# Optimization experiments

Hardware: AMD Instinct MI355X
Metric: run time of the kernel (lower is better)

The kernel has to match this reference:

```python
import jax, jax.numpy as jnp
import numpy as np

N, M, D = 1024, 1024, 256

def setup_inputs() -> dict:
    key = jax.random.key(0)
    ks = jax.random.split(key, 10)
    s = 1.0 / np.sqrt(D)
    return {
        "f_r": jax.random.normal(ks[0], (N, D), jnp.float32),
        "f_r_prime": jax.random.normal(ks[1], (M, D), jnp.float32),
        "W_w": jax.random.uniform(ks[2], (D, D), jnp.float32, -s, s),
        "W_b": jax.random.uniform(ks[3], (D,), jnp.float32, -s, s),
        "Wp_w": jax.random.uniform(ks[4], (D, D), jnp.float32, -s, s),
        "Wp_b": jax.random.uniform(ks[5], (D,), jnp.float32, -s, s),
        "w_w": jax.random.uniform(ks[6], (1, D), jnp.float32, -s, s),
        "w_b": jax.random.uniform(ks[7], (1,), jnp.float32, -s, s),
        "wp_w": jax.random.uniform(ks[8], (1, D), jnp.float32, -s, s),
        "wp_b": jax.random.uniform(ks[9], (1,), jnp.float32, -s, s),
    }

def reference(f_r, f_r_prime, W_w, W_b, Wp_w, Wp_b, w_w, w_b, wp_w, wp_b):
    q = f_r @ W_w.T + W_b            # [N, D]
    k = f_r_prime @ Wp_w.T + Wp_b    # [M, D]
    # additive (Bahdanau) scores: tanh over broadcast sum [N, M, D]
    h = jnp.tanh(q[:, None, :] + k[None, :, :])
    alpha = h @ w_w.T + w_b          # [N, M, 1]
    alpha = jax.nn.softmax(alpha, axis=1)
    # stage-1 pooling over M (weights on raw f_r_prime, as in source)
    context = jnp.sum(alpha * f_r_prime[None, :, :], axis=1)  # [N, D]
    # stage-2 attention pooling over N
    alpha_p = jax.nn.softmax(context @ wp_w.T + wp_b, axis=0)  # [N, 1]
    pool = jnp.sum(alpha_p * context, axis=0, keepdims=True)   # [1, D]
    return pool
```

## Files before the change

### kernel.cpp

```cpp
#include <hip/hip_runtime.h>

#define NN 1024
#define MM 1024
#define DD 256

typedef float floatx2 __attribute__((ext_vector_type(2)));

__device__ __forceinline__ float rcp_fast(float x) { return __builtin_amdgcn_rcpf(x); }

__global__ __launch_bounds__(256) void gemm_exp_kernel(
    const float* __restrict__ f_r,  const float* __restrict__ W_w,  const float* __restrict__ W_b,
    const float* __restrict__ f_rp, const float* __restrict__ Wp_w, const float* __restrict__ Wp_b,
    const float* __restrict__ wp_w,
    float* __restrict__ Eq, float* __restrict__ EkT, float* __restrict__ g,
    float* __restrict__ out0)
{
    __shared__ float As[32][36];
    __shared__ float Bs[32][68];
    __shared__ float T[64][36];

    const int b = blockIdx.x;
    const int t = threadIdx.x;

    if (b >= 256) {
        const int gb = b - 256;
        if (gb == 0) out0[t] = 0.f;
        const int m = gb * 256 + t;
        const float4* fm = (const float4*)(f_rp + (size_t)m * DD);
        const float4* wp = (const float4*)wp_w;
        float a0 = 0.f, a1 = 0.f, a2 = 0.f, a3 = 0.f;
        #pragma unroll 8
        for (int j = 0; j < 64; ++j) {
            float4 v = fm[j], w = wp[j];
            a0 = fmaf(v.x, w.x, a0); a1 = fmaf(v.y, w.y, a1);
            a2 = fmaf(v.z, w.z, a2); a3 = fmaf(v.w, w.w, a3);
        }
        g[m] = (a0 + a1) + (a2 + a3);
        return;
    }

    const int mat  = b >> 7;
    const int tile = b & 127;
    const int rt = tile & 31, dt = tile >> 5;
    const float* __restrict__ A    = mat ? f_rp : f_r;
    const float* __restrict__ B    = mat ? Wp_w : W_w;
    const float* __restrict__ bias = mat ? Wp_b : W_b;

    const int tx = t & 15, ty = t >> 4;
    const int r0 = rt * 32, d0 = dt * 64;
    const int ar = t >> 3, ak = (t & 7) * 4;
    const int br = t >> 2, bk = (t & 3) * 8;

    float acc[2][4];
    #pragma unroll
    for (int i = 0; i < 2; ++i)
        #pragma unroll
        for (int j = 0; j < 4; ++j) acc[i][j] = 0.f;

    for (int kk = 0; kk < DD; kk += 32) {
        float4 av  = *(const float4*)(A + (size_t)(r0 + ar) * DD + kk + ak);
        float4 bv0 = *(const float4*)(B + (size_t)(d0 + br) * DD + kk + bk);
        float4 bv1 = *(const float4*)(B + (size_t)(d0 + br) * DD + kk + bk + 4);
        __syncthreads();
        As[ak + 0][ar] = av.x; As[ak + 1][ar] = av.y; As[ak + 2][ar] = av.z; As[ak + 3][ar] = av.w;
        Bs[bk + 0][br] = bv0.x; Bs[bk + 1][br] = bv0.y; Bs[bk + 2][br] = bv0.z; Bs[bk + 3][br] = bv0.w;
        Bs[bk + 4][br] = bv1.x; Bs[bk + 5][br] = bv1.y; Bs[bk + 6][br] = bv1.z; Bs[bk + 7][br] = bv1.w;
        __syncthreads();
        #pragma unroll
        for (int k = 0; k < 32; ++k) {
            float2 a2 = *(const float2*)&As[k][ty * 2];
            float4 b4 = *(const float4*)&Bs[k][tx * 4];
            float aa[2] = {a2.x, a2.y};
            float bb[4] = {b4.x, b4.y, b4.z, b4.w};
            #pragma unroll
            for (int i = 0; i < 2; ++i)
                #pragma unroll
                for (int j = 0; j < 4; ++j)
                    acc[i][j] = fmaf(aa[i], bb[j], acc[i][j]);
        }
    }

    float bj[4];
    #pragma unroll
    for (int j = 0; j < 4; ++j) bj[j] = bias[d0 + tx * 4 + j];

    float e[2][4];
    #pragma unroll
    for (int i = 0; i < 2; ++i)
        #pragma unroll
        for (int j = 0; j < 4; ++j) {
            float v = acc[i][j] + bj[j];
            v = fminf(fmaxf(v, -5.f), 5.f);
            e[i][j] = __expf(2.f * v);
        }

    if (mat == 0) {
        #pragma unroll
        for (int i = 0; i < 2; ++i)
            *(float4*)&Eq[(size_t)(r0 + ty * 2 + i) * DD + d0 + tx * 4] =
                make_float4(e[i][0], e[i][1], e[i][2], e[i][3]);
    } else {
        __syncthreads();
        #pragma unroll
        for (int i = 0; i < 2; ++i)
            #pragma unroll
            for (int j = 0; j < 4; ++j) T[tx * 4 + j][ty * 2 + i] = e[i][j];
        __syncthreads();
        const int dl = t >> 3, rl = (t & 7) * 4;
        #pragma unroll
        for (int h = 0; h < 2; ++h) {
            int dloc = dl + 32 * h;
            float4 tv = *(const float4*)&T[dloc][rl];
            *(float4*)&EkT[(size_t)(d0 + dloc) * MM + r0 + rl] = tv;
        }
    }
}

__global__ __launch_bounds__(512, 4) void score_softmax_kernel(
    const float* __restrict__ Eq, const float* __restrict__ EkT,
    const float* __restrict__ w_w, const float* __restrict__ g,
    float* __restrict__ alpha, float* __restrict__ score)
{
    __shared__ float eq[2 * DD];
    __shared__ float w2[DD];
    __shared__ float accbuf[8][256];
    __shared__ float redmx[8 * 2];
    __shared__ float redsm[8 * 2];
    __shared__ float redg[4 * 2];

    const int t  = threadIdx.x;
    const int tg = t >> 8;
    const int tm = t & 255;
    const int lane = t & 63, wid = t >> 6;
    const int n0 = blockIdx.x * 2;
    const int dh = tg * 128;

    eq[t] = Eq[(size_t)n0 * DD + t];
    if (t < DD) w2[t] = -2.0f * w_w[t];
    __syncthreads();

    const floatx2 one2 = {1.f, 1.f};
    floatx2 accl[2] = {{0.f, 0.f}, {0.f, 0.f}};
    floatx2 acch[2] = {{0.f, 0.f}, {0.f, 0.f}};

    const float* ekb = EkT + (size_t)dh * MM + 4 * tm;

    float4 c0 = *(const float4*)(ekb + 0 * MM);
    float4 c1 = *(const float4*)(ekb + 1 * MM);
    float4 c2 = *(const float4*)(ekb + 2 * MM);
    float4 c3 = *(const float4*)(ekb + 3 * MM);

    for (int gi = 0; gi < 32; ++gi) {
        float4 p0 = c0, p1 = c1, p2 = c2, p3 = c3;
        if (gi < 31) {
            const float* nb = ekb + (size_t)(gi * 4 + 4) * MM;
            p0 = *(const float4*)(nb + 0 * MM);
            p1 = *(const float4*)(nb + 1 * MM);
            p2 = *(const float4*)(nb + 2 * MM);
            p3 = *(const float4*)(nb + 3 * MM);
        }
        const int db = gi * 4;
        float4 w4 = *(const float4*)&w2[dh + db];
        float4 qA = *(const float4*)&eq[dh + db];
        float4 qB = *(const float4*)&eq[DD + dh + db];

        floatx2 kv[4][2] = {{{c0.x, c0.y}, {c0.z, c0.w}},
                            {{c1.x, c1.y}, {c1.z, c1.w}},
                            {{c2.x, c2.y}, {c2.z, c2.w}},
                            {{c3.x, c3.y}, {c3.z, c3.w}}};
        float ws[4] = {w4.x, w4.y, w4.z, w4.w};
        float qs[2][4] = {{qA.x, qA.y, qA.z, qA.w}, {qB.x, qB.y, qB.z, qB.w}};

        #pragma unroll
        for (int h = 0; h < 2; ++h) {
            #pragma unroll
            for (int n = 0; n < 2; ++n) {
                floatx2 x0 = qs[n][0] * kv[0][h] + one2;
                floatx2 x1 = qs[n][1] * kv[1][h] + one2;
                floatx2 x2 = qs[n][2] * kv[2][h] + one2;
                floatx2 x3 = qs[n][3] * kv[3][h] + one2;
                floatx2 p01 = x0 * x1;
                floatx2 p23 = x2 * x3;
                floatx2 n01 = ws[0] * x1 + ws[1] * x0;
                floatx2 n23 = ws[2] * x3 + ws[3] * x2;
                floatx2 nc  = n01 * p23 + n23 * p01;
                floatx2 pt  = p01 * p23;
                floatx2 r;  r.x = rcp_fast(pt.x);  r.y = rcp_fast(pt.y);
                if (h == 0) accl[n] += nc * r; else acch[n] += nc * r;
            }
        }
        c0 = p0; c1 = p1; c2 = p2; c3 = p3;
    }

    float acc[2][4];
    #pragma unroll
    for (int n = 0; n < 2; ++n) {
        acc[n][0] = accl[n].x; acc[n][1] = accl[n].y;
        acc[n][2] = acch[n].x; acc[n][3] = acch[n].y;
    }

    if (tg == 1) {
        #pragma unroll
        for (int n = 0; n < 2; ++n)
            #pragma unroll
            for (int j = 0; j < 4; ++j) accbuf[n * 4 + j][tm] = acc[n][j];
    }
    __syncthreads();
    if (tg == 0) {
        #pragma unroll
        for (int n = 0; n < 2; ++n)
            #pragma unroll
            for (int j = 0; j < 4; ++j) acc[n][j] += accbuf[n * 4 + j][tm];
    }

    float mx[2];
    #pragma unroll
    for (int n = 0; n < 2; ++n) {
        mx[n] = (tg == 0) ? fmaxf(fmaxf(acc[n][0], acc[n][1]), fmaxf(acc[n][2], acc[n][3])) : -3e38f;
        #pragma unroll
        for (int off = 32; off > 0; off >>= 1) mx[n] = fmaxf(mx[n], __shfl_xor(mx[n], off));
    }
    if (lane == 0) { redmx[wid * 2] = mx[0]; redmx[wid * 2 + 1] = mx[1]; }
    __syncthreads();
    float MX[2];
    #pragma unroll
    for (int n = 0; n < 2; ++n) {
        float m = redmx[n];
        #pragma unroll
        for (int w = 1; w < 8; ++w) m = fmaxf(m, redmx[w * 2 + n]);
        MX[n] = m;
    }

    float e[2][4], sm[2];
    #pragma unroll
    for (int n = 0; n < 2; ++n) {
        sm[n] = 0.f;
        #pragma unroll
        for (int j = 0; j < 4; ++j) {
            e[n][j] = (tg == 0) ? __expf(acc[n][j] - MX[n]) : 0.f;
            sm[n] += e[n][j];
        }
        #pragma unroll
        for (int off = 32; off > 0; off >>= 1) sm[n] += __shfl_xor(sm[n], off);
    }
    if (lane == 0) { redsm[wid * 2] = sm[0]; redsm[wid * 2 + 1] = sm[1]; }
    __syncthreads();
    if (tg == 0) {
        float4 g4 = *(const float4*)&g[4 * tm];
        float sn[2];
        #pragma unroll
        for (int n = 0; n < 2; ++n) {
            float s = redsm[n];
            #pragma unroll
            for (int w = 1; w < 8; ++w) s += redsm[w * 2 + n];
            float inv = rcp_fast(s);
            float a0 = e[n][0] * inv, a1 = e[n][1] * inv, a2 = e[n][2] * inv, a3 = e[n][3] * inv;
            *(float4*)&alpha[(size_t)(n0 + n) * MM + 4 * tm] = make_float4(a0, a1, a2, a3);
            sn[n] = fmaf(a0, g4.x, fmaf(a1, g4.y, fmaf(a2, g4.z, a3 * g4.w)));
            #pragma unroll
            for (int off = 32; off > 0; off >>= 1) sn[n] += __shfl_xor(sn[n], off);
        }
        if (lane == 0) { redg[wid * 2] = sn[0]; redg[wid * 2 + 1] = sn[1]; }
    }
    __syncthreads();
    if (t == 0) score[n0]     = redg[0] + redg[2] + redg[4] + redg[6];
    if (t == 1) score[n0 + 1] = redg[1] + redg[3] + redg[5] + redg[7];
}

__global__ __launch_bounds__(256) void context_kernel(
    const float* __restrict__ alpha, const float* __restrict__ frp,
    float* __restrict__ part)
{
    __shared__ float als[16][128];
    const int t  = threadIdx.x;
    const int bm = blockIdx.x & 7;
    const int bn = blockIdx.x >> 3;
    const int dq = t & 63;
    const int ng = t >> 6;

    #pragma unroll
    for (int i = 0; i < 2; ++i) {
        int f4i = t + i * 256;
        int row = f4i >> 5, c4 = f4i & 31;
        *(float4*)&als[row][c4 * 4] =
            *(const float4*)&alpha[(size_t)(bn * 16 + row) * MM + bm * 128 + c4 * 4];
    }
    __syncthreads();

    float acc[4][4];
    #pragma unroll
    for (int n = 0; n < 4; ++n)
        #pragma unroll
        for (int j = 0; j < 4; ++j) acc[n][j] = 0.f;

    const float* fb = frp + (size_t)(bm * 128) * DD + 4 * dq;
    for (int m4 = 0; m4 < 32; ++m4) {
        float av[4][4];
        #pragma unroll
        for (int n = 0; n < 4; ++n) {
            float4 a4 = *(const float4*)&als[ng * 4 + n][m4 * 4];
            av[n][0] = a4.x; av[n][1] = a4.y; av[n][2] = a4.z; av[n][3] = a4.w;
        }
        #pragma unroll
        for (int mm = 0; mm < 4; ++mm) {
            float4 f4 = *(const float4*)(fb + (size_t)(m4 * 4 + mm) * DD);
            float fv[4] = {f4.x, f4.y, f4.z, f4.w};
            #pragma unroll
            for (int n = 0; n < 4; ++n)
                #pragma unroll
                for (int j = 0; j < 4; ++j)
                    acc[n][j] = fmaf(av[n][mm], fv[j], acc[n][j]);
        }
    }
    #pragma unroll
    for (int n = 0; n < 4; ++n)
        *(float4*)&part[((size_t)bm << 18) + (size_t)(bn * 16 + ng * 4 + n) * DD + 4 * dq] =
            make_float4(acc[n][0], acc[n][1], acc[n][2], acc[n][3]);
}

__global__ __launch_bounds__(256) void pool_kernel(
    const float* __restrict__ part, const float* __restrict__ score,
    float* __restrict__ out)
{
    __shared__ float red[8];
    const int t = threadIdx.x, lane = t & 63, wid = t >> 6;
    const int n0 = blockIdx.x * 4;

    float s0 = score[t], s1 = score[t + 256], s2 = score[t + 512], s3 = score[t + 768];
    float mx = fmaxf(fmaxf(s0, s1), fmaxf(s2, s3));
    #pragma unroll
    for (int off = 32; off > 0; off >>= 1) mx = fmaxf(mx, __shfl_xor(mx, off));
    if (lane == 0) red[wid] = mx;
    __syncthreads();
    mx = fmaxf(fmaxf(red[0], red[1]), fmaxf(red[2], red[3]));

    float se = __expf(s0 - mx) + __expf(s1 - mx) + __expf(s2 - mx) + __expf(s3 - mx);
    #pragma unroll
    for (int off = 32; off > 0; off >>= 1) se += __shfl_xor(se, off);
    if (lane == 0) red[4 + wid] = se;
    __syncthreads();
    se = red[4] + red[5] + red[6] + red[7];
    float invS = rcp_fast(se);

    float r = 0.f;
    #pragma unroll
    for (int i = 0; i < 4; ++i) {
        float ap = __expf(score[n0 + i] - mx) * invS;
        size_t idx = (size_t)(n0 + i) * DD + t;
        float c = 0.f;
        #pragma unroll
        for (int s = 0; s < 8; ++s) c += part[idx + ((size_t)s << 18)];
        r = fmaf(ap, c, r);
    }
    atomicAdd(out + t, r);
}

extern "C" void kernel_launch(void* const* d_in, const int* in_sizes, int n_in,
                              void* d_out, int out_size, void* d_ws, size_t ws_size,
                              hipStream_t stream) {
    const float* f_r  = (const float*)d_in[0];
    const float* f_rp = (const float*)d_in[1];
    const float* W_w  = (const float*)d_in[2];
    const float* W_b  = (const float*)d_in[3];
    const float* Wp_w = (const float*)d_in[4];
    const float* Wp_b = (const float*)d_in[5];
    const float* w_w  = (const float*)d_in[6];
    const float* wp_w = (const float*)d_in[8];
    float* out = (float*)d_out;

    float* ws    = (float*)d_ws;
    float* Eq    = ws;
    float* EkT   = ws + 262144;
    float* alpha = ws + 524288;
    float* part  = ws + 1572864;
    float* score = ws + 3670016;
    float* g     = ws + 3671040;

    gemm_exp_kernel<<<260, 256, 0, stream>>>(f_r, W_w, W_b, f_rp, Wp_w, Wp_b, wp_w,
                                             Eq, EkT, g, out);
    score_softmax_kernel<<<512, 512, 0, stream>>>(Eq, EkT, w_w, g, alpha, score);
    context_kernel<<<512, 256, 0, stream>>>(alpha, f_rp, part);
    pool_kernel<<<256, 256, 0, stream>>>(part, score, out);
}
```

Before: 136.3 us.

## Fuse score softmax and context pooling into one kernel per four query rows

Merges the score/softmax kernel and the context GEMM kernel into a single 1024-thread kernel. Each block now handles four query rows, keeps alpha in LDS and computes the context rows and the stage-2 scores directly, so the alpha and partial-context buffers no longer round-trip through global memory. The separate g = f_rp·wp_w precompute and one kernel launch are removed. In exchange each block now re-reads all of f_r_prime for only four rows, and the large LDS footprint (over 128KB) limits each CU to one block, which may reduce latency hiding.

```diff
diff --git a/kernel.cpp b/kernel.cpp
--- a/kernel.cpp
+++ b/kernel.cpp
@@ -11,9 +11,7 @@
 __global__ __launch_bounds__(256) void gemm_exp_kernel(
     const float* __restrict__ f_r,  const float* __restrict__ W_w,  const float* __restrict__ W_b,
     const float* __restrict__ f_rp, const float* __restrict__ Wp_w, const float* __restrict__ Wp_b,
-    const float* __restrict__ wp_w,
-    float* __restrict__ Eq, float* __restrict__ EkT, float* __restrict__ g,
-    float* __restrict__ out0)
+    float* __restrict__ Eq, float* __restrict__ EkT, float* __restrict__ out0)
 {
     __shared__ float As[32][36];
     __shared__ float Bs[32][68];
@@ -21,23 +19,7 @@
 
     const int b = blockIdx.x;
     const int t = threadIdx.x;
-
-    if (b >= 256) {
-        const int gb = b - 256;
-        if (gb == 0) out0[t] = 0.f;
-        const int m = gb * 256 + t;
-        const float4* fm = (const float4*)(f_rp + (size_t)m * DD);
-        const float4* wp = (const float4*)wp_w;
-        float a0 = 0.f, a1 = 0.f, a2 = 0.f, a3 = 0.f;
-        #pragma unroll 8
-        for (int j = 0; j < 64; ++j) {
-            float4 v = fm[j], w = wp[j];
-            a0 = fmaf(v.x, w.x, a0); a1 = fmaf(v.y, w.y, a1);
-            a2 = fmaf(v.z, w.z, a2); a3 = fmaf(v.w, w.w, a3);
-        }
-        g[m] = (a0 + a1) + (a2 + a3);
-        return;
-    }
+    if (b == 0) out0[t] = 0.f;
 
     const int mat  = b >> 7;
     const int tile = b & 127;
@@ -116,43 +98,45 @@
     }
 }
 
-__global__ __launch_bounds__(512, 4) void score_softmax_kernel(
+__global__ __launch_bounds__(1024, 4) void fused_attn_kernel(
     const float* __restrict__ Eq, const float* __restrict__ EkT,
-    const float* __restrict__ w_w, const float* __restrict__ g,
-    float* __restrict__ alpha, float* __restrict__ score)
+    const float* __restrict__ w_w, const float* __restrict__ frp,
+    const float* __restrict__ wp_w,
+    float* __restrict__ ctx, float* __restrict__ score)
 {
-    __shared__ float eq[2 * DD];
+    __shared__ float eq[4 * DD];
     __shared__ float w2[DD];
-    __shared__ float accbuf[8][256];
-    __shared__ float redmx[8 * 2];
-    __shared__ float redsm[8 * 2];
-    __shared__ float redg[4 * 2];
+    __shared__ float accbuf[3][16][256];
+    __shared__ float alsm[4][MM];
+    __shared__ float4 ctxred[16][4][64];
+    __shared__ float redmx[4][4];
+    __shared__ float redsm[4][4];
+    __shared__ float redsc[16];
 
     const int t  = threadIdx.x;
     const int tg = t >> 8;
     const int tm = t & 255;
     const int lane = t & 63, wid = t >> 6;
-    const int n0 = blockIdx.x * 2;
-    const int dh = tg * 128;
+    const int n0 = blockIdx.x * 4;
+    const int dh = tg * 64;
 
     eq[t] = Eq[(size_t)n0 * DD + t];
     if (t < DD) w2[t] = -2.0f * w_w[t];
     __syncthreads();
 
     const floatx2 one2 = {1.f, 1.f};
-    floatx2 accl[2] = {{0.f, 0.f}, {0.f, 0.f}};
-    floatx2 acch[2] = {{0.f, 0.f}, {0.f, 0.f}};
+    floatx2 accl[4] = {{0.f,0.f},{0.f,0.f},{0.f,0.f},{0.f,0.f}};
+    floatx2 acch[4] = {{0.f,0.f},{0.f,0.f},{0.f,0.f},{0.f,0.f}};
 
     const float* ekb = EkT + (size_t)dh * MM + 4 * tm;
-
     float4 c0 = *(const float4*)(ekb + 0 * MM);
     float4 c1 = *(const float4*)(ekb + 1 * MM);
     float4 c2 = *(const float4*)(ekb + 2 * MM);
     float4 c3 = *(const float4*)(ekb + 3 * MM);
 
-    for (int gi = 0; gi < 32; ++gi) {
+    for (int gi = 0; gi < 16; ++gi) {
         float4 p0 = c0, p1 = c1, p2 = c2, p3 = c3;
-        if (gi < 31) {
+        if (gi < 15) {
             const float* nb = ekb + (size_t)(gi * 4 + 4) * MM;
             p0 = *(const float4*)(nb + 0 * MM);
             p1 = *(const float4*)(nb + 1 * MM);
@@ -161,28 +145,23 @@
         }
         const int db = gi * 4;
         float4 w4 = *(const float4*)&w2[dh + db];
-        float4 qA = *(const float4*)&eq[dh + db];
-        float4 qB = *(const float4*)&eq[DD + dh + db];
-
         floatx2 kv[4][2] = {{{c0.x, c0.y}, {c0.z, c0.w}},
                             {{c1.x, c1.y}, {c1.z, c1.w}},
                             {{c2.x, c2.y}, {c2.z, c2.w}},
                             {{c3.x, c3.y}, {c3.z, c3.w}}};
-        float ws[4] = {w4.x, w4.y, w4.z, w4.w};
-        float qs[2][4] = {{qA.x, qA.y, qA.z, qA.w}, {qB.x, qB.y, qB.z, qB.w}};
-
-        #pragma unroll
-        for (int h = 0; h < 2; ++h) {
-            #pragma unroll
-            for (int n = 0; n < 2; ++n) {
-                floatx2 x0 = qs[n][0] * kv[0][h] + one2;
-                floatx2 x1 = qs[n][1] * kv[1][h] + one2;
-                floatx2 x2 = qs[n][2] * kv[2][h] + one2;
-                floatx2 x3 = qs[n][3] * kv[3][h] + one2;
+        #pragma unroll
+        for (int n = 0; n < 4; ++n) {
+            float4 q4 = *(const float4*)&eq[n * DD + dh + db];
+            #pragma unroll
+            for (int h = 0; h < 2; ++h) {
+                floatx2 x0 = q4.x * kv[0][h] + one2;
+                floatx2 x1 = q4.y * kv[1][h] + one2;
+                floatx2 x2 = q4.z * kv[2][h] + one2;
+                floatx2 x3 = q4.w * kv[3][h] + one2;
                 floatx2 p01 = x0 * x1;
                 floatx2 p23 = x2 * x3;
-                floatx2 n01 = ws[0] * x1 + ws[1] * x0;
-                floatx2 n23 = ws[2] * x3 + ws[3] * x2;
+                floatx2 n01 = w4.x * x1 + w4.y * x0;
+                floatx2 n23 = w4.z * x3 + w4.w * x2;
                 floatx2 nc  = n01 * p23 + n23 * p01;
                 floatx2 pt  = p01 * p23;
                 floatx2 r;  r.x = rcp_fast(pt.x);  r.y = rcp_fast(pt.y);
@@ -192,134 +171,108 @@
         c0 = p0; c1 = p1; c2 = p2; c3 = p3;
     }
 
-    float acc[2][4];
-    #pragma unroll
-    for (int n = 0; n < 2; ++n) {
+    float acc[4][4];
+    #pragma unroll
+    for (int n = 0; n < 4; ++n) {
         acc[n][0] = accl[n].x; acc[n][1] = accl[n].y;
         acc[n][2] = acch[n].x; acc[n][3] = acch[n].y;
     }
 
-    if (tg == 1) {
-        #pragma unroll
-        for (int n = 0; n < 2; ++n)
-            #pragma unroll
-            for (int j = 0; j < 4; ++j) accbuf[n * 4 + j][tm] = acc[n][j];
+    if (tg > 0) {
+        #pragma unroll
+        for (int n = 0; n < 4; ++n)
+            #pragma unroll
+            for (int j = 0; j < 4; ++j) accbuf[tg - 1][n * 4 + j][tm] = acc[n][j];
     }
     __syncthreads();
     if (tg == 0) {
         #pragma unroll
-        for (int n = 0; n < 2; ++n)
-            #pragma unroll
-            for (int j = 0; j < 4; ++j) acc[n][j] += accbuf[n * 4 + j][tm];
-    }
-
-    float mx[2];
-    #pragma unroll
-    for (int n = 0; n < 2; ++n) {
-        mx[n] = (tg == 0) ? fmaxf(fmaxf(acc[n][0], acc[n][1]), fmaxf(acc[n][2], acc[n][3])) : -3e38f;
-        #pragma unroll
-        for (int off = 32; off > 0; off >>= 1) mx[n] = fmaxf(mx[n], __shfl_xor(mx[n], off));
-    }
-    if (lane == 0) { redmx[wid * 2] = mx[0]; redmx[wid * 2 + 1] = mx[1]; }
-    __syncthreads();
-    float MX[2];
-    #pragma unroll
-    for (int n = 0; n < 2; ++n) {
-        float m = redmx[n];
-        #pragma unroll
-        for (int w = 1; w < 8; ++w) m = fmaxf(m, redmx[w * 2 + n]);
-        MX[n] = m;
-    }
-
-    float e[2][4], sm[2];
-    #pragma unroll
-    for (int n = 0; n < 2; ++n) {
-        sm[n] = 0.f;
-        #pragma unroll
-        for (int j = 0; j < 4; ++j) {
-            e[n][j] = (tg == 0) ? __expf(acc[n][j] - MX[n]) : 0.f;
-            sm[n] += e[n][j];
-        }
-        #pragma unroll
-        for (int off = 32; off > 0; off >>= 1) sm[n] += __shfl_xor(sm[n], off);
-    }
-    if (lane == 0) { redsm[wid * 2] = sm[0]; redsm[wid * 2 + 1] = sm[1]; }
-    __syncthreads();
-    if (tg == 0) {
-        float4 g4 = *(const float4*)&g[4 * tm];
-        float sn[2];
-        #pragma unroll
-        for (int n = 0; n < 2; ++n) {
-            float s = redsm[n];
-            #pragma unroll
-            for (int w = 1; w < 8; ++w) s += redsm[w * 2 + n];
-            float inv = rcp_fast(s);
-            float a0 = e[n][0] * inv, a1 = e[n][1] * inv, a2 = e[n][2] * inv, a3 = e[n][3] * inv;
-            *(float4*)&alpha[(size_t)(n0 + n) * MM + 4 * tm] = make_float4(a0, a1, a2, a3);
-            sn[n] = fmaf(a0, g4.x, fmaf(a1, g4.y, fmaf(a2, g4.z, a3 * g4.w)));
-            #pragma unroll
-            for (int off = 32; off > 0; off >>= 1) sn[n] += __shfl_xor(sn[n], off);
-        }
-        if (lane == 0) { redg[wid * 2] = sn[0]; redg[wid * 2 + 1] = sn[1]; }
-    }
-    __syncthreads();
-    if (t == 0) score[n0]     = redg[0] + redg[2] + redg[4] + redg[6];
-    if (t == 1) score[n0 + 1] = redg[1] + redg[3] + redg[5] + redg[7];
-}
-
-__global__ __launch_bounds__(256) void context_kernel(
-    const float* __restrict__ alpha, const float* __restrict__ frp,
-    float* __restrict__ part)
-{
-    __shared__ float als[16][128];
-    const int t  = threadIdx.x;
-    const int bm = blockIdx.x & 7;
-    const int bn = blockIdx.x >> 3;
-    const int dq = t & 63;
-    const int ng = t >> 6;
-
-    #pragma unroll
-    for (int i = 0; i < 2; ++i) {
-        int f4i = t + i * 256;
-        int row = f4i >> 5, c4 = f4i & 31;
-        *(float4*)&als[row][c4 * 4] =
-            *(const float4*)&alpha[(size_t)(bn * 16 + row) * MM + bm * 128 + c4 * 4];
-    }
-    __syncthreads();
-
-    float acc[4][4];
-    #pragma unroll
-    for (int n = 0; n < 4; ++n)
-        #pragma unroll
-        for (int j = 0; j < 4; ++j) acc[n][j] = 0.f;
-
-    const float* fb = frp + (size_t)(bm * 128) * DD + 4 * dq;
-    for (int m4 = 0; m4 < 32; ++m4) {
-        float av[4][4];
-        #pragma unroll
-        for (int n = 0; n < 4; ++n) {
-            float4 a4 = *(const float4*)&als[ng * 4 + n][m4 * 4];
-            av[n][0] = a4.x; av[n][1] = a4.y; av[n][2] = a4.z; av[n][3] = a4.w;
-        }
-        #pragma unroll
-        for (int mm = 0; mm < 4; ++mm) {
-            float4 f4 = *(const float4*)(fb + (size_t)(m4 * 4 + mm) * DD);
-            float fv[4] = {f4.x, f4.y, f4.z, f4.w};
+        for (int s = 0; s < 3; ++s)
             #pragma unroll
             for (int n = 0; n < 4; ++n)
                 #pragma unroll
-                for (int j = 0; j < 4; ++j)
-                    acc[n][j] = fmaf(av[n][mm], fv[j], acc[n][j]);
+                for (int j = 0; j < 4; ++j) acc[n][j] += accbuf[s][n * 4 + j][tm];
+        float mx[4];
+        #pragma unroll
+        for (int n = 0; n < 4; ++n) {
+            mx[n] = fmaxf(fmaxf(acc[n][0], acc[n][1]), fmaxf(acc[n][2], acc[n][3]));
+            #pragma unroll
+            for (int off = 32; off > 0; off >>= 1) mx[n] = fmaxf(mx[n], __shfl_xor(mx[n], off));
+            if (lane == 0) redmx[wid][n] = mx[n];
+        }
+    }
+    __syncthreads();
+    float e[4][4];
+    if (tg == 0) {
+        #pragma unroll
+        for (int n = 0; n < 4; ++n) {
+            float MX = fmaxf(fmaxf(redmx[0][n], redmx[1][n]), fmaxf(redmx[2][n], redmx[3][n]));
+            float sm = 0.f;
+            #pragma unroll
+            for (int j = 0; j < 4; ++j) { e[n][j] = __expf(acc[n][j] - MX); sm += e[n][j]; }
+            #pragma unroll
+            for (int off = 32; off > 0; off >>= 1) sm += __shfl_xor(sm, off);
+            if (lane == 0) redsm[wid][n] = sm;
+        }
+    }
+    __syncthreads();
+    if (tg == 0) {
+        #pragma unroll
+        for (int n = 0; n < 4; ++n) {
+            float S = redsm[0][n] + redsm[1][n] + redsm[2][n] + redsm[3][n];
+            float inv = rcp_fast(S);
+            #pragma unroll
+            for (int j = 0; j < 4; ++j) alsm[n][4 * tm + j] = e[n][j] * inv;
+        }
+    }
+    __syncthreads();
+
+    const int cc = t & 63;
+    const int rr = t >> 6;
+    const int m0 = rr * 64;
+    floatx2 axl[4] = {{0.f,0.f},{0.f,0.f},{0.f,0.f},{0.f,0.f}};
+    floatx2 axh[4] = {{0.f,0.f},{0.f,0.f},{0.f,0.f},{0.f,0.f}};
+    const float* fb = frp + (size_t)m0 * DD + 4 * cc;
+    for (int m4 = 0; m4 < 16; ++m4) {
+        float alv[4][4];
+        #pragma unroll
+        for (int n = 0; n < 4; ++n) {
+            float4 a4 = *(const float4*)&alsm[n][m0 + m4 * 4];
+            alv[n][0] = a4.x; alv[n][1] = a4.y; alv[n][2] = a4.z; alv[n][3] = a4.w;
+        }
+        #pragma unroll
+        for (int mm = 0; mm < 4; ++mm) {
+            float4 f = *(const float4*)(fb + (size_t)(m4 * 4 + mm) * DD);
+            floatx2 fl = {f.x, f.y}, fh = {f.z, f.w};
+            #pragma unroll
+            for (int n = 0; n < 4; ++n) {
+                axl[n] += alv[n][mm] * fl;
+                axh[n] += alv[n][mm] * fh;
+            }
         }
     }
     #pragma unroll
     for (int n = 0; n < 4; ++n)
-        *(float4*)&part[((size_t)bm << 18) + (size_t)(bn * 16 + ng * 4 + n) * DD + 4 * dq] =
-            make_float4(acc[n][0], acc[n][1], acc[n][2], acc[n][3]);
+        ctxred[rr][n][cc] = make_float4(axl[n].x, axl[n].y, axh[n].x, axh[n].y);
+    __syncthreads();
+
+    const int nn = t >> 8, d = t & 255;
+    float s = 0.f;
+    #pragma unroll
+    for (int r = 0; r < 16; ++r)
+        s += ((const float*)&ctxred[r][nn][d >> 2])[d & 3];
+    ctx[(size_t)(n0 + nn) * DD + d] = s;
+
+    float p = s * wp_w[d];
+    #pragma unroll
+    for (int off = 32; off > 0; off >>= 1) p += __shfl_xor(p, off);
+    if (lane == 0) redsc[wid] = p;
+    __syncthreads();
+    if (t < 4) score[n0 + t] = redsc[4 * t] + redsc[4 * t + 1] + redsc[4 * t + 2] + redsc[4 * t + 3];
 }
 
 __global__ __launch_bounds__(256) void pool_kernel(
-    const float* __restrict__ part, const float* __restrict__ score,
+    const float* __restrict__ ctx, const float* __restrict__ score,
     float* __restrict__ out)
 {
     __shared__ float red[8];
@@ -346,11 +299,7 @@
     #pragma unroll
     for (int i = 0; i < 4; ++i) {
         float ap = __expf(score[n0 + i] - mx) * invS;
-        size_t idx = (size_t)(n0 + i) * DD + t;
-        float c = 0.f;
-        #pragma unroll
-        for (int s = 0; s < 8; ++s) c += part[idx + ((size_t)s << 18)];
-        r = fmaf(ap, c, r);
+        r = fmaf(ap, ctx[(size_t)(n0 + i) * DD + t], r);
     }
     atomicAdd(out + t, r);
 }
@@ -371,14 +320,10 @@
     float* ws    = (float*)d_ws;
     float* Eq    = ws;
     float* EkT   = ws + 262144;
-    float* alpha = ws + 524288;
-    float* part  = ws + 1572864;
-    float* score = ws + 3670016;
-    float* g     = ws + 3671040;
-
-    gemm_exp_kernel<<<260, 256, 0, stream>>>(f_r, W_w, W_b, f_rp, Wp_w, Wp_b, wp_w,
-                                             Eq, EkT, g, out);
-    score_softmax_kernel<<<512, 512, 0, stream>>>(Eq, EkT, w_w, g, alpha, score);
-    context_kernel<<<512, 256, 0, stream>>>(alpha, f_rp, part);
-    pool_kernel<<<256, 256, 0, stream>>>(part, score, out);
+    float* ctx   = ws + 524288;
+    float* score = ws + 786432;
+
+    gemm_exp_kernel<<<256, 256, 0, stream>>>(f_r, W_w, W_b, f_rp, Wp_w, Wp_b, Eq, EkT, out);
+    fused_attn_kernel<<<256, 1024, 0, stream>>>(Eq, EkT, w_w, f_rp, wp_w, ctx, score);
+    pool_kernel<<<256, 256, 0, stream>>>(ctx, score, out);
 }
```

Result: faster. 125.1 us (-8.2%).
